# Optimization experiments

Measured on AMD Instinct MI355X. Metric: run time of the kernel, lower is better.

The kernel has to match this reference:

```python
import jax, jax.numpy as jnp
import numpy as np

HIDDEN = 1024
BETA = 1.0
SPARSITY_THRESHOLD = 1.0


def _sparsemax(x):
    # Faithful port of the module's custom sparsemax (including its
    # nonstandard per-position tau). Operates over the last axis.
    n = x.shape[-1]
    z = x - jnp.max(x, axis=-1, keepdims=True)
    sum_z = jnp.sum(z, axis=-1, keepdims=True)
    step = (sum_z - 1.0) / n                       # step_size
    sorted_z = -jnp.sort(-z, axis=-1)              # descending sort
    cumsum_z = jnp.cumsum(sorted_z, axis=-1)
    is_gt = sorted_z > step
    rng = jnp.arange(1, n + 1, dtype=jnp.int32)
    k = jnp.max(rng * is_gt, axis=-1, keepdims=True).astype(x.dtype)
    tau = (cumsum_z - 1.0 - step * k) / k          # [.., n] per-position tau
    return jnp.clip(z - tau, 0.0)


def setup_inputs() -> dict:
    key = jax.random.key(0)
    kx, kq, kk, kv = jax.random.split(key, 4)
    B, S, D = 4, 2048, 1024
    x = jax.random.normal(kx, (B, S, D), dtype=jnp.float32)
    # torch Linear weight layout: [out_features, in_features]
    scale = 1.0 / np.sqrt(D)
    Wq = jax.random.normal(kq, (HIDDEN, D), dtype=jnp.float32) * scale
    Wk = jax.random.normal(kk, (HIDDEN, D), dtype=jnp.float32) * scale
    Wv = jax.random.normal(kv, (HIDDEN, D), dtype=jnp.float32) * scale
    return {"x": x, "Wq": Wq, "Wk": Wk, "Wv": Wv}


def reference(x, Wq, Wk, Wv):
    Q = jnp.einsum('bsd,hd->bsh', x, Wq)
    K = jnp.einsum('bsd,hd->bsh', x, Wk)
    V = jnp.einsum('bsd,hd->bsh', x, Wv)
    energy = jnp.einsum('bsh,bth->bst', Q, K) / jnp.sqrt(jnp.asarray(HIDDEN, x.dtype))
    scores = energy * BETA
    sparsity = jnp.mean(jnp.abs(x))
    attention = jax.lax.cond(
        sparsity < SPARSITY_THRESHOLD,
        _sparsemax,
        lambda s: jax.nn.softmax(s, axis=-1),
        scores,
    )
    return jnp.einsum('bst,bth->bsh', attention, V)
```

## Files before the change

kernel.cpp:

```cpp
#include <hip/hip_runtime.h>
#include <math.h>

#define B_   4
#define S_   2048
#define D_   1024
#define H_   1024
#define NROW 2048
#define TOTX 8388608.0f

typedef _Float16 f16x8 __attribute__((ext_vector_type(8)));
typedef float f32x4 __attribute__((ext_vector_type(4)));

__device__ __forceinline__ unsigned short f2h(float f) {
  _Float16 h = (_Float16)f;
  return __builtin_bit_cast(unsigned short, h);
}

#define GLD16(gp, lp)                                                            \
  __builtin_amdgcn_global_load_lds(                                              \
      (__attribute__((address_space(1))) void*)(gp),                             \
      (__attribute__((address_space(3))) void*)(lp), 16, 0, 0)

__global__ __launch_bounds__(256) void f2h_abs_kernel(const float* __restrict__ in,
                                                      unsigned short* __restrict__ out,
                                                      float* absOut, int n4) {
  int i0 = blockIdx.x * 256 + threadIdx.x;
  int stride = gridDim.x * 256;
  float s = 0.f;
  for (int i = i0; i < n4; i += stride) {
    float4 v = ((const float4*)in)[i];
    ushort4 o;
    o.x = f2h(v.x); o.y = f2h(v.y); o.z = f2h(v.z); o.w = f2h(v.w);
    ((ushort4*)out)[i] = o;
    s += fabsf(v.x) + fabsf(v.y) + fabsf(v.z) + fabsf(v.w);
  }
#pragma unroll
  for (int off = 32; off; off >>= 1) s += __shfl_xor(s, off);
  __shared__ float red[4];
  if ((threadIdx.x & 63) == 0) red[threadIdx.x >> 6] = s;
  __syncthreads();
  if (threadIdx.x == 0) atomicAdd(absOut, red[0] + red[1] + red[2] + red[3]);
}

__global__ __launch_bounds__(256) void f2h3_kernel(const float* __restrict__ a,
                                                   const float* __restrict__ b,
                                                   const float* __restrict__ c,
                                                   unsigned short* __restrict__ oa,
                                                   unsigned short* __restrict__ ob,
                                                   unsigned short* __restrict__ oc,
                                                   int n4) {
  int i = blockIdx.x * 256 + threadIdx.x;
  if (i >= n4) return;
  const float* in = (blockIdx.y == 0) ? a : (blockIdx.y == 1) ? b : c;
  unsigned short* out = (blockIdx.y == 0) ? oa : (blockIdx.y == 1) ? ob : oc;
  float4 v = ((const float4*)in)[i];
  ushort4 o;
  o.x = f2h(v.x); o.y = f2h(v.y); o.z = f2h(v.z); o.w = f2h(v.w);
  ((ushort4*)out)[i] = o;
}

__global__ __launch_bounds__(256) void transpose_h16(const unsigned short* __restrict__ in,
                                                     unsigned short* __restrict__ out,
                                                     int R, int C) {
  __shared__ unsigned short t[32][33];
  const int z = blockIdx.z;
  in  += (long long)z * R * C;
  out += (long long)z * R * C;
  const int c0 = blockIdx.x * 32, r0 = blockIdx.y * 32;
#pragma unroll
  for (int i = 0; i < 4; ++i) {
    int r = threadIdx.y + i * 8;
    t[r][threadIdx.x] = in[(long long)(r0 + r) * C + c0 + threadIdx.x];
  }
  __syncthreads();
#pragma unroll
  for (int i = 0; i < 4; ++i) {
    int r = threadIdx.y + i * 8;
    out[(long long)(c0 + r) * R + r0 + threadIdx.x] = t[threadIdx.x][r];
  }
}

template <bool OUT_F16>
__global__ __launch_bounds__(512, 2) void gemm8_nt(const unsigned short* __restrict__ A,
                                                   const unsigned short* __restrict__ B,
                                                   void* __restrict__ Cv,
                                                   int M, int N, int K,
                                                   long long sA, long long sB, long long sC,
                                                   float scale) {
  const int bz = blockIdx.z;
  A += (long long)bz * sA;
  B += (long long)bz * sB;

  __shared__ __align__(16) unsigned short lds[2][2][8192];

  const int tid = threadIdx.x;
  const int lane = tid & 63;
  const int w = tid >> 6;
  const int wr = w >> 2;
  const int wc = w & 3;
  const int m0 = blockIdx.y * 256, n0 = blockIdx.x * 256;

  f32x4 acc[8][4] = {};

  const int srow = w * 16 + (lane >> 2);
  const int scol = ((lane & 3) ^ ((lane >> 3) & 3)) * 8;
  const unsigned short* gA0 = A + (long long)(m0 + srow) * K + scol;
  const unsigned short* gA1 = gA0 + (long long)128 * K;
  const unsigned short* gB0 = B + (long long)(n0 + srow) * K + scol;
  const unsigned short* gB1 = gB0 + (long long)128 * K;
  const int wb = w * 512;

  const int fm = lane & 15;
  const int col8 = ((lane >> 4) ^ ((lane >> 1) & 3)) * 8;
  int aoff[8], boff[4];
#pragma unroll
  for (int mi = 0; mi < 8; ++mi) aoff[mi] = (wr * 128 + mi * 16 + fm) * 32 + col8;
#pragma unroll
  for (int ni = 0; ni < 4; ++ni) boff[ni] = (wc * 64 + ni * 16 + fm) * 32 + col8;

  const int nt = K >> 5;

#define STAGE8(nb, k0)                                   \
  do {                                                   \
    GLD16(gA0 + (k0), &lds[nb][0][wb]);                  \
    GLD16(gA1 + (k0), &lds[nb][0][4096 + wb]);           \
    GLD16(gB0 + (k0), &lds[nb][1][wb]);                  \
    GLD16(gB1 + (k0), &lds[nb][1][4096 + wb]);           \
  } while (0)

  STAGE8(0, 0);
  asm volatile("s_waitcnt vmcnt(0)" ::: "memory");
  __builtin_amdgcn_s_barrier();

  for (int t = 0; t < nt; ++t) {
    const int cur = t & 1;
    const unsigned short* Ar = lds[cur][0];
    const unsigned short* Br = lds[cur][1];
    if (t + 1 < nt) {
      const int k1 = (t + 1) << 5;
      if (cur) STAGE8(0, k1); else STAGE8(1, k1);
    }
    f16x8 af[4], bf[4];
#pragma unroll
    for (int mi = 0; mi < 4; ++mi) af[mi] = *(const f16x8*)(Ar + aoff[mi]);
#pragma unroll
    for (int ni = 0; ni < 4; ++ni) bf[ni] = *(const f16x8*)(Br + boff[ni]);
    __builtin_amdgcn_s_barrier();
    asm volatile("s_waitcnt lgkmcnt(0)" ::: "memory");
    __builtin_amdgcn_sched_barrier(0);
    __builtin_amdgcn_s_setprio(1);
#pragma unroll
    for (int mi = 0; mi < 4; ++mi)
#pragma unroll
      for (int ni = 0; ni < 4; ++ni)
        acc[mi][ni] = __builtin_amdgcn_mfma_f32_16x16x32_f16(af[mi], bf[ni],
                                                             acc[mi][ni], 0, 0, 0);
    __builtin_amdgcn_s_setprio(0);
    __builtin_amdgcn_s_barrier();
    f16x8 ag[4];
#pragma unroll
    for (int mi = 0; mi < 4; ++mi) ag[mi] = *(const f16x8*)(Ar + aoff[mi + 4]);
    __builtin_amdgcn_s_barrier();
    asm volatile("s_waitcnt lgkmcnt(0)" ::: "memory");
    __builtin_amdgcn_sched_barrier(0);
    __builtin_amdgcn_s_setprio(1);
#pragma unroll
    for (int mi = 0; mi < 4; ++mi)
#pragma unroll
      for (int ni = 0; ni < 4; ++ni)
        acc[mi + 4][ni] = __builtin_amdgcn_mfma_f32_16x16x32_f16(ag[mi], bf[ni],
                                                                 acc[mi + 4][ni], 0, 0, 0);
    __builtin_amdgcn_s_setprio(0);
    if (t + 1 < nt) asm volatile("s_waitcnt vmcnt(0)" ::: "memory");
    __builtin_amdgcn_s_barrier();
  }
#undef STAGE8

  const int cm = (lane >> 4) * 4;
  const int cn = lane & 15;
#pragma unroll
  for (int mi = 0; mi < 8; ++mi)
#pragma unroll
    for (int ni = 0; ni < 4; ++ni) {
#pragma unroll
      for (int r = 0; r < 4; ++r) {
        long long m = m0 + wr * 128 + mi * 16 + cm + r;
        long long n = n0 + wc * 64 + ni * 16 + cn;
        float v = acc[mi][ni][r] * scale;
        if (OUT_F16)
          ((unsigned short*)Cv)[(long long)bz * sC + m * N + n] = f2h(v);
        else
          ((float*)Cv)[(long long)bz * sC + m * N + n] = v;
      }
    }
}

template <int K, int J>
__device__ __forceinline__ void intra_s(float (&r)[32]) {
#pragma unroll
  for (int v = 0; v < 32; ++v)
    if ((v & J) == 0) {
      const int u = v | J;
      const bool dsc = ((v & K) == 0);
      float a = r[v], b = r[u];
      float mx = fmaxf(a, b), mn = fminf(a, b);
      r[v] = dsc ? mx : mn;
      r[u] = dsc ? mn : mx;
    }
}

template <int J>
__device__ __forceinline__ void intra_desc(float (&r)[32]) {
#pragma unroll
  for (int v = 0; v < 32; ++v)
    if ((v & J) == 0) {
      const int u = v | J;
      float a = r[v], b = r[u];
      r[v] = fmaxf(a, b);
      r[u] = fminf(a, b);
    }
}

template <int JL>
__device__ __forceinline__ void cross_desc(float (&r)[32], int lane, int bp32) {
  const bool keepmax = ((lane & JL) == 0);
  float b[32];
#pragma unroll
  for (int v = 0; v < 32; ++v) {
    int av = __builtin_bit_cast(int, r[v]);
    int bv;
    if constexpr (JL == 32)
      bv = __builtin_amdgcn_ds_bpermute(bp32, av);
    else
      bv = __builtin_amdgcn_ds_swizzle(av, (JL << 10) | 0x1F);
    b[v] = __builtin_bit_cast(float, bv);
  }
#pragma unroll
  for (int v = 0; v < 32; ++v) {
    float mx = fmaxf(r[v], b[v]), mn = fminf(r[v], b[v]);
    r[v] = keepmax ? mx : mn;
  }
}

__device__ __forceinline__ void signfix(float (&r)[32], unsigned fix) {
#pragma unroll
  for (int v = 0; v < 32; ++v)
    r[v] = __builtin_bit_cast(float, __builtin_bit_cast(unsigned, r[v]) ^ fix);
}

__global__ __launch_bounds__(256, 4) void attn_row_wave(const float* __restrict__ scores,
                                                        unsigned short* __restrict__ attn,
                                                        const float* __restrict__ absSum) {
  __shared__ float zs[4][2048];
  const int tid = threadIdx.x;
  const int lane = tid & 63;
  const int wv = tid >> 6;
  const int row = blockIdx.x * 4 + wv;
  const float* rowp = scores + (long long)row * NROW;
  unsigned short* aout = attn + (long long)row * NROW;
  float* zrow = zs[wv];
  const int bp32 = (lane ^ 32) << 2;

  float lm = -INFINITY;
#pragma unroll
  for (int q = 0; q < 8; ++q) {
    float4 v = ((const float4*)rowp)[q * 64 + lane];
    int chunk = q * 64 + lane;
    int swz = (chunk & ~7) | ((chunk ^ (chunk >> 3)) & 7);
    ((float4*)zrow)[swz] = v;
    lm = fmaxf(lm, fmaxf(fmaxf(v.x, v.y), fmaxf(v.z, v.w)));
  }
#pragma unroll
  for (int off = 32; off; off >>= 1) lm = fmaxf(lm, __shfl_xor(lm, off, 64));
  __syncthreads();

  const bool use_softmax = (absSum[0] * (1.0f / TOTX)) >= 1.0f;

  if (use_softmax) {
    float z[32];
    float ls = 0.f;
#pragma unroll
    for (int q = 0; q < 8; ++q) {
      int swz = lane * 8 + (q ^ (lane & 7));
      float4 v = ((const float4*)zrow)[swz];
      z[q * 4 + 0] = expf(v.x - lm); z[q * 4 + 1] = expf(v.y - lm);
      z[q * 4 + 2] = expf(v.z - lm); z[q * 4 + 3] = expf(v.w - lm);
      ls += z[q * 4 + 0] + z[q * 4 + 1] + z[q * 4 + 2] + z[q * 4 + 3];
    }
#pragma unroll
    for (int off = 32; off; off >>= 1) ls += __shfl_xor(ls, off, 64);
    float inv = 1.0f / ls;
    ushort4* op = (ushort4*)(aout + lane * 32);
#pragma unroll
    for (int q = 0; q < 8; ++q) {
      ushort4 o;
      o.x = f2h(z[q * 4 + 0] * inv); o.y = f2h(z[q * 4 + 1] * inv);
      o.z = f2h(z[q * 4 + 2] * inv); o.w = f2h(z[q * 4 + 3] * inv);
      op[q] = o;
    }
    return;
  }

  float r[32];
  float lsum = 0.f;
#pragma unroll
  for (int q = 0; q < 8; ++q) {
    int swz = lane * 8 + (q ^ (lane & 7));
    float4 v = ((const float4*)zrow)[swz];
    r[q * 4 + 0] = v.x - lm; r[q * 4 + 1] = v.y - lm;
    r[q * 4 + 2] = v.z - lm; r[q * 4 + 3] = v.w - lm;
    lsum += r[q * 4 + 0] + r[q * 4 + 1] + r[q * 4 + 2] + r[q * 4 + 3];
  }
#pragma unroll
  for (int off = 32; off; off >>= 1) lsum += __shfl_xor(lsum, off, 64);
  const float step = (lsum - 1.0f) * (1.0f / (float)NROW);

  intra_s<2, 1>(r);
  intra_s<4, 2>(r); intra_s<4, 1>(r);
  intra_s<8, 4>(r); intra_s<8, 2>(r); intra_s<8, 1>(r);
  intra_s<16, 8>(r); intra_s<16, 4>(r); intra_s<16, 2>(r); intra_s<16, 1>(r);

  unsigned cur = (unsigned)(lane & 1) << 31;
  signfix(r, cur);
  intra_desc<16>(r); intra_desc<8>(r); intra_desc<4>(r);
  intra_desc<2>(r); intra_desc<1>(r);

  { unsigned want = (unsigned)(lane & 2) << 30;
    signfix(r, cur ^ want); cur = want; }
  cross_desc<1>(r, lane, bp32);
  intra_desc<16>(r); intra_desc<8>(r); intra_desc<4>(r);
  intra_desc<2>(r); intra_desc<1>(r);

  { unsigned want = (unsigned)(lane & 4) << 29;
    signfix(r, cur ^ want); cur = want; }
  cross_desc<2>(r, lane, bp32); cross_desc<1>(r, lane, bp32);
  intra_desc<16>(r); intra_desc<8>(r); intra_desc<4>(r);
  intra_desc<2>(r); intra_desc<1>(r);

  { unsigned want = (unsigned)(lane & 8) << 28;
    signfix(r, cur ^ want); cur = want; }
  cross_desc<4>(r, lane, bp32); cross_desc<2>(r, lane, bp32);
  cross_desc<1>(r, lane, bp32);
  intra_desc<16>(r); intra_desc<8>(r); intra_desc<4>(r);
  intra_desc<2>(r); intra_desc<1>(r);

  { unsigned want = (unsigned)(lane & 16) << 27;
    signfix(r, cur ^ want); cur = want; }
  cross_desc<8>(r, lane, bp32); cross_desc<4>(r, lane, bp32);
  cross_desc<2>(r, lane, bp32); cross_desc<1>(r, lane, bp32);
  intra_desc<16>(r); intra_desc<8>(r); intra_desc<4>(r);
  intra_desc<2>(r); intra_desc<1>(r);

  { unsigned want = (unsigned)(lane & 32) << 26;
    signfix(r, cur ^ want); cur = want; }
  cross_desc<16>(r, lane, bp32); cross_desc<8>(r, lane, bp32);
  cross_desc<4>(r, lane, bp32); cross_desc<2>(r, lane, bp32);
  cross_desc<1>(r, lane, bp32);
  intra_desc<16>(r); intra_desc<8>(r); intra_desc<4>(r);
  intra_desc<2>(r); intra_desc<1>(r);

  signfix(r, cur);
  cross_desc<32>(r, lane, bp32); cross_desc<16>(r, lane, bp32);
  cross_desc<8>(r, lane, bp32); cross_desc<4>(r, lane, bp32);
  cross_desc<2>(r, lane, bp32); cross_desc<1>(r, lane, bp32);
  intra_desc<16>(r); intra_desc<8>(r); intra_desc<4>(r);
  intra_desc<2>(r); intra_desc<1>(r);

  float lcnt = 0.f;
#pragma unroll
  for (int v = 0; v < 32; ++v) lcnt += (r[v] > step) ? 1.0f : 0.0f;
#pragma unroll
  for (int off = 32; off; off >>= 1) lcnt += __shfl_xor(lcnt, off, 64);
  const float kf = lcnt;

  float run = 0.f;
#pragma unroll
  for (int v = 0; v < 32; ++v) { run += r[v]; r[v] = run; }
  float pre = run;
#pragma unroll
  for (int off = 1; off < 64; off <<= 1) {
    float t = __shfl_up(pre, off, 64);
    if (lane >= off) pre += t;
  }
  pre -= run;
#pragma unroll
  for (int v = 0; v < 32; ++v) r[v] += pre;

  const float inv_k = 1.0f / kf;
  const float c1 = 1.0f + step * kf;
  ushort4* op = (ushort4*)(aout + lane * 32);
#pragma unroll
  for (int q = 0; q < 8; ++q) {
    int swz = lane * 8 + (q ^ (lane & 7));
    float4 v = ((const float4*)zrow)[swz];
    ushort4 o;
    o.x = f2h(fmaxf((v.x - lm) - (r[q * 4 + 0] - c1) * inv_k, 0.0f));
    o.y = f2h(fmaxf((v.y - lm) - (r[q * 4 + 1] - c1) * inv_k, 0.0f));
    o.z = f2h(fmaxf((v.z - lm) - (r[q * 4 + 2] - c1) * inv_k, 0.0f));
    o.w = f2h(fmaxf((v.w - lm) - (r[q * 4 + 3] - c1) * inv_k, 0.0f));
    op[q] = o;
  }
}

extern "C" void kernel_launch(void* const* d_in, const int* in_sizes, int n_in,
                              void* d_out, int out_size, void* d_ws, size_t ws_size,
                              hipStream_t stream) {
  const float* x  = (const float*)d_in[0];
  const float* Wq = (const float*)d_in[1];
  const float* Wk = (const float*)d_in[2];
  const float* Wv = (const float*)d_in[3];
  float* out = (float*)d_out;

  const long long NX = (long long)B_ * S_ * D_;
  const long long NW = (long long)H_ * D_;

  char* base = (char*)d_ws;
  unsigned short* x16  = (unsigned short*)(base);
  unsigned short* Wq16 = (unsigned short*)(base + (16ll << 20));
  unsigned short* Wk16 = (unsigned short*)(base + (18ll << 20));
  unsigned short* Wv16 = (unsigned short*)(base + (20ll << 20));
  float*          Sc   = (float*)(base);
  unsigned short* Vt16 = (unsigned short*)(base + (64ll << 20));
  unsigned short* Q16  = (unsigned short*)(base + (80ll << 20));
  unsigned short* K16  = (unsigned short*)(base + (96ll << 20));
  unsigned short* V16  = (unsigned short*)(base + (112ll << 20));
  unsigned short* A16  = (unsigned short*)(base + (80ll << 20));
  float*          flag = (float*)(base + (144ll << 20));

  hipMemsetAsync(flag, 0, sizeof(float), stream);

  f2h_abs_kernel<<<1024, 256, 0, stream>>>(x, x16, flag, (int)(NX / 4));
  f2h3_kernel<<<dim3((int)(NW / 4 + 255) / 256, 3), 256, 0, stream>>>(
      Wq, Wk, Wv, Wq16, Wk16, Wv16, (int)(NW / 4));

  {
    dim3 grid(H_ / 256, (B_ * S_) / 256, 3);
    gemm8_nt<true><<<grid, 512, 0, stream>>>(x16, Wq16, Q16, B_ * S_, H_, D_,
                                             0, (long long)NW, (long long)(8ll << 20),
                                             1.0f);
  }

  {
    dim3 grid(H_ / 32, S_ / 32, B_);
    transpose_h16<<<grid, dim3(32, 8), 0, stream>>>(V16, Vt16, S_, H_);
  }

  {
    dim3 grid(S_ / 256, S_ / 256, B_);
    gemm8_nt<false><<<grid, 512, 0, stream>>>(Q16, K16, Sc, S_, S_, H_,
                                              (long long)S_ * H_, (long long)S_ * H_,
                                              (long long)S_ * S_, 1.0f / 32.0f);
  }

  attn_row_wave<<<(B_ * S_) / 4, 256, 0, stream>>>(Sc, A16, flag);

  {
    dim3 grid(H_ / 256, S_ / 256, B_);
    gemm8_nt<false><<<grid, 512, 0, stream>>>(A16, Vt16, out, S_, H_, S_,
                                              (long long)S_ * S_, (long long)H_ * S_,
                                              (long long)S_ * H_, 1.0f);
  }
}
```

Before: 378.6 us.

## Triple-stage GEMM prefetch, smaller M tiles for skinny GEMMs, register-resident attention rows

The GEMM is templated on the M tile size. The QKV and AV GEMMs use 128-row tiles, which doubles the grid so more blocks are available to fill the CUs. The GEMM main loop now prefetches two K-steps ahead with partial vmcnt waits and drops several barriers per iteration, aiming to hide global-to-LDS latency. The attention row kernel no longer stages scores in LDS. It keeps the row in registers, computes the raw sum in the same pass as the max, and re-reads the scores from global memory for the final output, trading LDS traffic and a sync for a second global read.

```diff
diff --git a/kernel.cpp b/kernel.cpp
--- a/kernel.cpp
+++ b/kernel.cpp
@@ -80,29 +80,35 @@
   }
 }
 
-template <bool OUT_F16>
+template <int MI, bool OUT_F16>
 __global__ __launch_bounds__(512, 2) void gemm8_nt(const unsigned short* __restrict__ A,
                                                    const unsigned short* __restrict__ B,
                                                    void* __restrict__ Cv,
                                                    int M, int N, int K,
                                                    long long sA, long long sB, long long sC,
                                                    float scale) {
+  constexpr int BM  = MI * 32;
+  constexpr int ASZ = BM * 32;
+  constexpr int BSZ = 256 * 32;
+  constexpr int TSZ = ASZ + BSZ;
+  constexpr int MH  = MI / 2;
+
   const int bz = blockIdx.z;
   A += (long long)bz * sA;
   B += (long long)bz * sB;
 
-  __shared__ __align__(16) unsigned short lds[2][2][8192];
+  __shared__ __align__(16) unsigned short lds[2 * TSZ];
 
   const int tid = threadIdx.x;
   const int lane = tid & 63;
   const int w = tid >> 6;
   const int wr = w >> 2;
   const int wc = w & 3;
-  const int m0 = blockIdx.y * 256, n0 = blockIdx.x * 256;
-
-  f32x4 acc[8][4] = {};
-
-  const int srow = w * 16 + (lane >> 2);
+  const int m0 = blockIdx.y * BM, n0 = blockIdx.x * 256;
+
+  f32x4 acc[MI][4] = {};
+
+  const int srow = tid >> 2;
   const int scol = ((lane & 3) ^ ((lane >> 3) & 3)) * 8;
   const unsigned short* gA0 = A + (long long)(m0 + srow) * K + scol;
   const unsigned short* gA1 = gA0 + (long long)128 * K;
@@ -112,79 +118,78 @@
 
   const int fm = lane & 15;
   const int col8 = ((lane >> 4) ^ ((lane >> 1) & 3)) * 8;
-  int aoff[8], boff[4];
-#pragma unroll
-  for (int mi = 0; mi < 8; ++mi) aoff[mi] = (wr * 128 + mi * 16 + fm) * 32 + col8;
-#pragma unroll
-  for (int ni = 0; ni < 4; ++ni) boff[ni] = (wc * 64 + ni * 16 + fm) * 32 + col8;
+  int aoff[MI], boff[4];
+#pragma unroll
+  for (int mi = 0; mi < MI; ++mi) aoff[mi] = (wr * (MI * 16) + mi * 16 + fm) * 32 + col8;
+#pragma unroll
+  for (int ni = 0; ni < 4; ++ni) boff[ni] = ASZ + (wc * 64 + ni * 16 + fm) * 32 + col8;
 
   const int nt = K >> 5;
 
-#define STAGE8(nb, k0)                                   \
+#define STAGE(nb, k0)                                    \
   do {                                                   \
-    GLD16(gA0 + (k0), &lds[nb][0][wb]);                  \
-    GLD16(gA1 + (k0), &lds[nb][0][4096 + wb]);           \
-    GLD16(gB0 + (k0), &lds[nb][1][wb]);                  \
-    GLD16(gB1 + (k0), &lds[nb][1][4096 + wb]);           \
+    unsigned short* L_ = lds + (nb) * TSZ;               \
+    GLD16(gA0 + (k0), L_ + wb);                          \
+    if (MI == 8) GLD16(gA1 + (k0), L_ + 4096 + wb);      \
+    GLD16(gB0 + (k0), L_ + ASZ + wb);                    \
+    GLD16(gB1 + (k0), L_ + ASZ + 4096 + wb);             \
   } while (0)
 
-  STAGE8(0, 0);
-  asm volatile("s_waitcnt vmcnt(0)" ::: "memory");
+  STAGE(0, 0);
+  STAGE(1, 32);
+  if (MI == 8) asm volatile("s_waitcnt vmcnt(4)" ::: "memory");
+  else         asm volatile("s_waitcnt vmcnt(3)" ::: "memory");
   __builtin_amdgcn_s_barrier();
 
   for (int t = 0; t < nt; ++t) {
-    const int cur = t & 1;
-    const unsigned short* Ar = lds[cur][0];
-    const unsigned short* Br = lds[cur][1];
-    if (t + 1 < nt) {
-      const int k1 = (t + 1) << 5;
-      if (cur) STAGE8(0, k1); else STAGE8(1, k1);
-    }
-    f16x8 af[4], bf[4];
-#pragma unroll
-    for (int mi = 0; mi < 4; ++mi) af[mi] = *(const f16x8*)(Ar + aoff[mi]);
-#pragma unroll
-    for (int ni = 0; ni < 4; ++ni) bf[ni] = *(const f16x8*)(Br + boff[ni]);
-    __builtin_amdgcn_s_barrier();
-    asm volatile("s_waitcnt lgkmcnt(0)" ::: "memory");
-    __builtin_amdgcn_sched_barrier(0);
+    const unsigned short* L = lds + (t & 1) * TSZ;
+    f16x8 af[MH], bf[4];
+#pragma unroll
+    for (int mi = 0; mi < MH; ++mi) af[mi] = *(const f16x8*)(L + aoff[mi]);
+#pragma unroll
+    for (int ni = 0; ni < 4; ++ni) bf[ni] = *(const f16x8*)(L + boff[ni]);
     __builtin_amdgcn_s_setprio(1);
 #pragma unroll
-    for (int mi = 0; mi < 4; ++mi)
+    for (int mi = 0; mi < MH; ++mi)
 #pragma unroll
       for (int ni = 0; ni < 4; ++ni)
         acc[mi][ni] = __builtin_amdgcn_mfma_f32_16x16x32_f16(af[mi], bf[ni],
                                                              acc[mi][ni], 0, 0, 0);
     __builtin_amdgcn_s_setprio(0);
-    __builtin_amdgcn_s_barrier();
-    f16x8 ag[4];
-#pragma unroll
-    for (int mi = 0; mi < 4; ++mi) ag[mi] = *(const f16x8*)(Ar + aoff[mi + 4]);
-    __builtin_amdgcn_s_barrier();
+    f16x8 ag[MH];
+#pragma unroll
+    for (int mi = 0; mi < MH; ++mi) ag[mi] = *(const f16x8*)(L + aoff[MH + mi]);
     asm volatile("s_waitcnt lgkmcnt(0)" ::: "memory");
     __builtin_amdgcn_sched_barrier(0);
+    __builtin_amdgcn_s_barrier();
+    if (t + 2 < nt) STAGE(t & 1, (t + 2) << 5);
     __builtin_amdgcn_s_setprio(1);
 #pragma unroll
-    for (int mi = 0; mi < 4; ++mi)
+    for (int mi = 0; mi < MH; ++mi)
 #pragma unroll
       for (int ni = 0; ni < 4; ++ni)
-        acc[mi + 4][ni] = __builtin_amdgcn_mfma_f32_16x16x32_f16(ag[mi], bf[ni],
-                                                                 acc[mi + 4][ni], 0, 0, 0);
+        acc[MH + mi][ni] = __builtin_amdgcn_mfma_f32_16x16x32_f16(ag[mi], bf[ni],
+                                                                  acc[MH + mi][ni], 0, 0, 0);
     __builtin_amdgcn_s_setprio(0);
-    if (t + 1 < nt) asm volatile("s_waitcnt vmcnt(0)" ::: "memory");
+    if (t + 2 < nt) {
+      if (MI == 8) asm volatile("s_waitcnt vmcnt(4)" ::: "memory");
+      else         asm volatile("s_waitcnt vmcnt(3)" ::: "memory");
+    } else if (t + 1 < nt) {
+      asm volatile("s_waitcnt vmcnt(0)" ::: "memory");
+    }
     __builtin_amdgcn_s_barrier();
   }
-#undef STAGE8
+#undef STAGE
 
   const int cm = (lane >> 4) * 4;
   const int cn = lane & 15;
 #pragma unroll
-  for (int mi = 0; mi < 8; ++mi)
+  for (int mi = 0; mi < MI; ++mi)
 #pragma unroll
     for (int ni = 0; ni < 4; ++ni) {
 #pragma unroll
       for (int r = 0; r < 4; ++r) {
-        long long m = m0 + wr * 128 + mi * 16 + cm + r;
+        long long m = m0 + wr * (MI * 16) + mi * 16 + cm + r;
         long long n = n0 + wc * 64 + ni * 16 + cn;
         float v = acc[mi][ni][r] * scale;
         if (OUT_F16)
@@ -235,6 +240,7 @@
       bv = __builtin_amdgcn_ds_swizzle(av, (JL << 10) | 0x1F);
     b[v] = __builtin_bit_cast(float, bv);
   }
+  __builtin_amdgcn_sched_barrier(0);
 #pragma unroll
   for (int v = 0; v < 32; ++v) {
     float mx = fmaxf(r[v], b[v]), mn = fminf(r[v], b[v]);
@@ -251,42 +257,36 @@
 __global__ __launch_bounds__(256, 4) void attn_row_wave(const float* __restrict__ scores,
                                                         unsigned short* __restrict__ attn,
                                                         const float* __restrict__ absSum) {
-  __shared__ float zs[4][2048];
   const int tid = threadIdx.x;
   const int lane = tid & 63;
-  const int wv = tid >> 6;
-  const int row = blockIdx.x * 4 + wv;
+  const int row = blockIdx.x * 4 + (tid >> 6);
   const float* rowp = scores + (long long)row * NROW;
   unsigned short* aout = attn + (long long)row * NROW;
-  float* zrow = zs[wv];
   const int bp32 = (lane ^ 32) << 2;
 
-  float lm = -INFINITY;
+  const float4* rp4 = (const float4*)rowp + lane * 8;
+  float r[32];
+  float lm = -INFINITY, lsraw = 0.f;
 #pragma unroll
   for (int q = 0; q < 8; ++q) {
-    float4 v = ((const float4*)rowp)[q * 64 + lane];
-    int chunk = q * 64 + lane;
-    int swz = (chunk & ~7) | ((chunk ^ (chunk >> 3)) & 7);
-    ((float4*)zrow)[swz] = v;
+    float4 v = rp4[q];
+    r[q * 4 + 0] = v.x; r[q * 4 + 1] = v.y;
+    r[q * 4 + 2] = v.z; r[q * 4 + 3] = v.w;
     lm = fmaxf(lm, fmaxf(fmaxf(v.x, v.y), fmaxf(v.z, v.w)));
-  }
-#pragma unroll
-  for (int off = 32; off; off >>= 1) lm = fmaxf(lm, __shfl_xor(lm, off, 64));
-  __syncthreads();
+    lsraw += v.x + v.y + v.z + v.w;
+  }
+#pragma unroll
+  for (int off = 32; off; off >>= 1) {
+    lm = fmaxf(lm, __shfl_xor(lm, off, 64));
+    lsraw += __shfl_xor(lsraw, off, 64);
+  }
 
   const bool use_softmax = (absSum[0] * (1.0f / TOTX)) >= 1.0f;
 
   if (use_softmax) {
-    float z[32];
     float ls = 0.f;
 #pragma unroll
-    for (int q = 0; q < 8; ++q) {
-      int swz = lane * 8 + (q ^ (lane & 7));
-      float4 v = ((const float4*)zrow)[swz];
-      z[q * 4 + 0] = expf(v.x - lm); z[q * 4 + 1] = expf(v.y - lm);
-      z[q * 4 + 2] = expf(v.z - lm); z[q * 4 + 3] = expf(v.w - lm);
-      ls += z[q * 4 + 0] + z[q * 4 + 1] + z[q * 4 + 2] + z[q * 4 + 3];
-    }
+    for (int v = 0; v < 32; ++v) { r[v] = expf(r[v] - lm); ls += r[v]; }
 #pragma unroll
     for (int off = 32; off; off >>= 1) ls += __shfl_xor(ls, off, 64);
     float inv = 1.0f / ls;
@@ -294,26 +294,16 @@
 #pragma unroll
     for (int q = 0; q < 8; ++q) {
       ushort4 o;
-      o.x = f2h(z[q * 4 + 0] * inv); o.y = f2h(z[q * 4 + 1] * inv);
-      o.z = f2h(z[q * 4 + 2] * inv); o.w = f2h(z[q * 4 + 3] * inv);
+      o.x = f2h(r[q * 4 + 0] * inv); o.y = f2h(r[q * 4 + 1] * inv);
+      o.z = f2h(r[q * 4 + 2] * inv); o.w = f2h(r[q * 4 + 3] * inv);
       op[q] = o;
     }
     return;
   }
 
-  float r[32];
-  float lsum = 0.f;
-#pragma unroll
-  for (int q = 0; q < 8; ++q) {
-    int swz = lane * 8 + (q ^ (lane & 7));
-    float4 v = ((const float4*)zrow)[swz];
-    r[q * 4 + 0] = v.x - lm; r[q * 4 + 1] = v.y - lm;
-    r[q * 4 + 2] = v.z - lm; r[q * 4 + 3] = v.w - lm;
-    lsum += r[q * 4 + 0] + r[q * 4 + 1] + r[q * 4 + 2] + r[q * 4 + 3];
-  }
-#pragma unroll
-  for (int off = 32; off; off >>= 1) lsum += __shfl_xor(lsum, off, 64);
-  const float step = (lsum - 1.0f) * (1.0f / (float)NROW);
+#pragma unroll
+  for (int v = 0; v < 32; ++v) r[v] -= lm;
+  const float step = ((lsraw - (float)NROW * lm) - 1.0f) * (1.0f / (float)NROW);
 
   intra_s<2, 1>(r);
   intra_s<4, 2>(r); intra_s<4, 1>(r);
@@ -388,11 +378,14 @@
 
   const float inv_k = 1.0f / kf;
   const float c1 = 1.0f + step * kf;
+
+  unsigned long long up = (unsigned long long)rowp;
+  asm volatile("" : "+v"(up));
+  const float4* rp4e = (const float4*)up + lane * 8;
   ushort4* op = (ushort4*)(aout + lane * 32);
 #pragma unroll
   for (int q = 0; q < 8; ++q) {
-    int swz = lane * 8 + (q ^ (lane & 7));
-    float4 v = ((const float4*)zrow)[swz];
+    float4 v = rp4e[q];
     ushort4 o;
     o.x = f2h(fmaxf((v.x - lm) - (r[q * 4 + 0] - c1) * inv_k, 0.0f));
     o.y = f2h(fmaxf((v.y - lm) - (r[q * 4 + 1] - c1) * inv_k, 0.0f));
@@ -434,10 +427,10 @@
       Wq, Wk, Wv, Wq16, Wk16, Wv16, (int)(NW / 4));
 
   {
-    dim3 grid(H_ / 256, (B_ * S_) / 256, 3);
-    gemm8_nt<true><<<grid, 512, 0, stream>>>(x16, Wq16, Q16, B_ * S_, H_, D_,
-                                             0, (long long)NW, (long long)(8ll << 20),
-                                             1.0f);
+    dim3 grid(H_ / 256, (B_ * S_) / 128, 3);
+    gemm8_nt<4, true><<<grid, 512, 0, stream>>>(x16, Wq16, Q16, B_ * S_, H_, D_,
+                                                0, (long long)NW, (long long)(8ll << 20),
+                                                1.0f);
   }
 
   {
@@ -447,17 +440,17 @@
 
   {
     dim3 grid(S_ / 256, S_ / 256, B_);
-    gemm8_nt<false><<<grid, 512, 0, stream>>>(Q16, K16, Sc, S_, S_, H_,
-                                              (long long)S_ * H_, (long long)S_ * H_,
-                                              (long long)S_ * S_, 1.0f / 32.0f);
+    gemm8_nt<8, false><<<grid, 512, 0, stream>>>(Q16, K16, Sc, S_, S_, H_,
+                                                 (long long)S_ * H_, (long long)S_ * H_,
+                                                 (long long)S_ * S_, 1.0f / 32.0f);
   }
 
   attn_row_wave<<<(B_ * S_) / 4, 256, 0, stream>>>(Sc, A16, flag);
 
   {
-    dim3 grid(H_ / 256, S_ / 256, B_);
-    gemm8_nt<false><<<grid, 512, 0, stream>>>(A16, Vt16, out, S_, H_, S_,
-                                              (long long)S_ * S_, (long long)H_ * S_,
-                                              (long long)S_ * H_, 1.0f);
-  }
-}
+    dim3 grid(H_ / 256, S_ / 128, B_);
+    gemm8_nt<4, false><<<grid, 512, 0, stream>>>(A16, Vt16, out, S_, H_, S_,
+                                                 (long long)S_ * S_, (long long)H_ * S_,
+                                                 (long long)S_ * H_, 1.0f);
+  }
+}
```

Result: faster. 338.0 us (-10.7%).
